# Performance work log

Measured on AMD Instinct MI355X. Metric: run time of the kernel, lower is better.

## Reference

```python
import jax, jax.numpy as jnp
import numpy as np

MARGIN = 1.0

def setup_inputs() -> dict:
    key = jax.random.key(0)
    k1, k2, k3 = jax.random.split(key, 3)
    B, C, D = 65536, 1000, 512
    x = jax.random.normal(k1, (B, D), dtype=jnp.float32)
    x = x / jnp.linalg.norm(x, axis=1, keepdims=True)  # docstring: ||x||2 = 1
    labels = jax.random.randint(k2, (B,), 0, C, dtype=jnp.int64)
    centers = jax.random.normal(k3, (C, D), dtype=jnp.float32)
    return {"x": x, "labels": labels, "centers": centers}

def reference(x, labels, centers):
    # l2Norm applied to the centers (module is only used when l2Norm is truthy)
    c = centers / jnp.linalg.norm(centers, axis=1, keepdims=True)  # (C, D)
    # cosine distance to every center: one batched GEMM instead of per-sample loop
    dist = 1.0 - jnp.einsum("bd,cd->bc", x, c)                      # (B, C)
    pos = jnp.take_along_axis(dist, labels[:, None], axis=1)[:, 0]  # (B,)
    # min over all classes != label: mask own class with +inf
    same = jnp.arange(c.shape[0])[None, :] == labels[:, None]       # (B, C)
    neg = jnp.min(jnp.where(same, jnp.inf, dist), axis=1)           # (B,)
    # sum of per-sample hinge losses divided by batch size == mean
    return jnp.mean(jax.nn.relu(pos + MARGIN - neg))
```

## Files before the change

kernel.cpp:

```cpp
#include <hip/hip_runtime.h>
#include <stdint.h>

typedef short v8s __attribute__((ext_vector_type(8)));
typedef short v4s __attribute__((ext_vector_type(4)));
typedef float v4f __attribute__((ext_vector_type(4)));

#define BM 256
#define BN 128
#define BKH 32
#define ASH (BM * BKH)
#define TSH ((BM + BN) * BKH)
#define POS_INF __builtin_inff()

typedef __attribute__((address_space(3))) unsigned int lds_uint;
typedef const __attribute__((address_space(1))) unsigned int glb_uint;

__device__ __forceinline__ void load16_lds(const void* g, void* l) {
    __builtin_amdgcn_global_load_lds((glb_uint*)g, (lds_uint*)l, 16, 0, 0);
}

__device__ __forceinline__ short f2bf(float f) {
    uint32_t u = __builtin_bit_cast(uint32_t, f);
    u += 0x7fffu + ((u >> 16) & 1u);
    return (short)(u >> 16);
}

__global__ void prep(const float* __restrict__ centers,
                     unsigned short* __restrict__ cbf,
                     int C, int D, int CP, int CB,
                     const float* __restrict__ x,
                     unsigned short* __restrict__ xbf, size_t nx,
                     int* __restrict__ cnt, int NB,
                     float* __restrict__ out) {
    const int b = blockIdx.x;
    const int t = threadIdx.x;
    if (b == 0 && t == 0) out[0] = 0.0f;
    if (b < CB) {
        const int g = b * 256 + t;
        if (g < NB) cnt[g] = 0;
        const int wave = t >> 6, lane = t & 63;
        const int row = b * 4 + wave;
        if (row >= CP) return;
        if (row >= C) {
            v4s z = {0, 0, 0, 0};
            for (int d = lane * 4; d < D; d += 256)
                *(v4s*)&cbf[(size_t)row * D + d] = z;
            return;
        }
        const float* src = centers + (size_t)row * D;
        float ss = 0.0f;
        for (int d = lane * 4; d < D; d += 256) {
            v4f f = *(const v4f*)&src[d];
            ss += f.x * f.x + f.y * f.y + f.z * f.z + f.w * f.w;
        }
        #pragma unroll
        for (int off = 32; off; off >>= 1) ss += __shfl_xor(ss, off, 64);
        const float rn = rsqrtf(ss);
        for (int d = lane * 4; d < D; d += 256) {
            v4f f = *(const v4f*)&src[d];
            v4s s;
            s.x = f2bf(f.x * rn); s.y = f2bf(f.y * rn);
            s.z = f2bf(f.z * rn); s.w = f2bf(f.w * rn);
            *(v4s*)&cbf[(size_t)row * D + d] = s;
        }
    } else {
        const size_t i = ((size_t)(b - CB) * 256 + t) * 8;
        if (i >= nx) return;
        v4f f0 = *(const v4f*)&x[i];
        v4f f1 = *(const v4f*)&x[i + 4];
        v8s s;
        s[0] = f2bf(f0.x); s[1] = f2bf(f0.y); s[2] = f2bf(f0.z); s[3] = f2bf(f0.w);
        s[4] = f2bf(f1.x); s[5] = f2bf(f1.y); s[6] = f2bf(f1.z); s[7] = f2bf(f1.w);
        *(v8s*)&xbf[i] = s;
    }
}

__global__ void __launch_bounds__(512)
gemm_fused(const unsigned short* __restrict__ xbf,
           const unsigned short* __restrict__ cbf,
           const int* __restrict__ labels,
           float* __restrict__ pos, float* __restrict__ partial,
           int* __restrict__ cnt,
           int Bt, int C, int D, int NT, float margin,
           float* __restrict__ out) {
    extern __shared__ short LDS[];

    const int t   = threadIdx.x;
    const int bid = blockIdx.x;
    const int xcd = bid & 7;
    const int per = bid >> 3;
    const int rowblk = (per >> 3) * 8 + xcd;
    const int nt     = per & 7;
    const int row0 = rowblk * BM;
    const int n0   = nt * BN;

    const int lane = t & 63;
    const int wave = t >> 6;
    const int wm = wave >> 1;
    const int wn = wave & 1;
    const int l15 = lane & 15, q = lane >> 4;

    const int rsub = lane >> 2;
    const int csrc = (lane & 3) ^ ((lane >> 3) & 3);

    int myLab = 0;
    if (t < BM) myLab = labels[row0 + t];

    v4f acc[4][4];
    #pragma unroll
    for (int i = 0; i < 4; ++i)
        #pragma unroll
        for (int j = 0; j < 4; ++j)
            acc[i][j] = (v4f){0.f, 0.f, 0.f, 0.f};

    #define WAITVM3() do { asm volatile("s_waitcnt vmcnt(3)" ::: "memory"); } while (0)
    #define WAITVM0() do { asm volatile("s_waitcnt vmcnt(0)" ::: "memory"); } while (0)
    #define BARRIER() do { __builtin_amdgcn_s_barrier(); \
                           __builtin_amdgcn_sched_barrier(0); } while (0)

    #define STAGE(buf_, k0_) do {                                            \
        load16_lds(&xbf[(size_t)(row0 + wave * 32 + rsub) * D + (k0_) + csrc * 8], \
                   &LDS[(buf_) + (wave * 32) * BKH]);                        \
        load16_lds(&xbf[(size_t)(row0 + wave * 32 + 16 + rsub) * D + (k0_) + csrc * 8], \
                   &LDS[(buf_) + (wave * 32 + 16) * BKH]);                   \
        load16_lds(&cbf[(size_t)(n0 + wave * 16 + rsub) * D + (k0_) + csrc * 8], \
                   &LDS[(buf_) + ASH + (wave * 16) * BKH]);                  \
    } while (0)

    #define TILE(buf_) do {                                                  \
        v8s a[4], b[4];                                                      \
        _Pragma("unroll")                                                    \
        for (int i = 0; i < 4; ++i)                                          \
            a[i] = *(const v8s*)&LDS[(buf_) + (wm * 64 + i * 16 + l15) * BKH \
                                     + ((q ^ ((l15 >> 1) & 3)) << 3)];       \
        _Pragma("unroll")                                                    \
        for (int j = 0; j < 4; ++j)                                          \
            b[j] = *(const v8s*)&LDS[(buf_) + ASH + (wn * 64 + j * 16 + l15) * BKH \
                                     + ((q ^ ((l15 >> 1) & 3)) << 3)];       \
        _Pragma("unroll")                                                    \
        for (int i = 0; i < 4; ++i)                                          \
            _Pragma("unroll")                                                \
            for (int j = 0; j < 4; ++j)                                      \
                acc[i][j] = __builtin_amdgcn_mfma_f32_16x16x32_bf16(         \
                    a[i], b[j], acc[i][j], 0, 0, 0);                         \
    } while (0)

    int bc = 0, b1 = TSH, b2 = 2 * TSH;

    STAGE(bc, 0);
    STAGE(b1, BKH);

    const int KT = D / BKH;
    for (int kt = 0; kt + 2 < KT; ++kt) {
        WAITVM3();
        BARRIER();
        STAGE(b2, (kt + 2) * BKH);
        TILE(bc);
        const int tmp = bc; bc = b1; b1 = b2; b2 = tmp;
    }
    WAITVM3();
    BARRIER();
    TILE(bc);
    WAITVM0();
    BARRIER();
    TILE(b1);

    #undef STAGE
    #undef TILE
    #undef WAITVM3
    #undef WAITVM0
    #undef BARRIER

    __syncthreads();

    int*   Ls    = (int*)LDS;
    float* sMinW = (float*)((char*)LDS + 1024);
    int*   sLast = (int*)((char*)LDS + 3072);
    float* wsum  = (float*)((char*)LDS + 3088);
    if (t < BM) Ls[t] = myLab;
    __syncthreads();

    #pragma unroll
    for (int i = 0; i < 4; ++i) {
        #pragma unroll
        for (int rg = 0; rg < 4; ++rg) {
            const int row_l = wm * 64 + i * 16 + q * 4 + rg;
            const int lab = Ls[row_l];
            float m = POS_INF;
            #pragma unroll
            for (int j = 0; j < 4; ++j) {
                const int col = n0 + wn * 64 + j * 16 + l15;
                const float d = 1.0f - acc[i][j][rg];
                if (col == lab)
                    __hip_atomic_store(&pos[row0 + row_l], d,
                                       __ATOMIC_RELAXED, __HIP_MEMORY_SCOPE_AGENT);
                else if (col < C) m = fminf(m, d);
            }
            m = fminf(m, __shfl_xor(m, 1, 64));
            m = fminf(m, __shfl_xor(m, 2, 64));
            m = fminf(m, __shfl_xor(m, 4, 64));
            m = fminf(m, __shfl_xor(m, 8, 64));
            if (l15 == 0) sMinW[wn * BM + row_l] = m;
        }
    }
    __syncthreads();
    if (t < BM) {
        const float m = fminf(sMinW[t], sMinW[BM + t]);
        __hip_atomic_store(&partial[(size_t)nt * Bt + row0 + t], m,
                           __ATOMIC_RELAXED, __HIP_MEMORY_SCOPE_AGENT);
    }
    __syncthreads();

    if (t == 0) {
        __builtin_amdgcn_s_waitcnt(0);
        const int old = __hip_atomic_fetch_add(&cnt[rowblk], 1,
                                               __ATOMIC_RELAXED,
                                               __HIP_MEMORY_SCOPE_AGENT);
        *sLast = (old == NT - 1);
    }
    __syncthreads();
    if (!*sLast) return;

    float hng = 0.0f;
    if (t < BM) {
        const int r = row0 + t;
        float neg = POS_INF;
        for (int tt = 0; tt < NT; ++tt)
            neg = fminf(neg, __hip_atomic_load(&partial[(size_t)tt * Bt + r],
                                               __ATOMIC_RELAXED,
                                               __HIP_MEMORY_SCOPE_AGENT));
        const float p = __hip_atomic_load(&pos[r], __ATOMIC_RELAXED,
                                          __HIP_MEMORY_SCOPE_AGENT);
        hng = fmaxf(0.0f, p + margin - neg);
    }
    #pragma unroll
    for (int off = 32; off; off >>= 1) hng += __shfl_down(hng, off, 64);
    if (lane == 0) wsum[wave] = hng;
    __syncthreads();
    if (t == 0) {
        float s = 0.0f;
        #pragma unroll
        for (int w = 0; w < 8; ++w) s += wsum[w];
        atomicAdd(out, s * (1.0f / (float)Bt));
    }
}

extern "C" void kernel_launch(void* const* d_in, const int* in_sizes, int n_in,
                              void* d_out, int out_size, void* d_ws, size_t ws_size,
                              hipStream_t stream) {
    const float* x       = (const float*)d_in[0];
    const int*   labels  = (const int*)d_in[1];
    const float* centers = (const float*)d_in[2];
    float* out = (float*)d_out;

    const int Bt = in_sizes[1];
    const int D  = in_sizes[0] / Bt;
    const int C  = in_sizes[2] / D;
    const int NT = (C + BN - 1) / BN;
    const int CP = NT * BN;
    const int NB = Bt / BM;

    char* ws = (char*)d_ws;
    unsigned short* cbf = (unsigned short*)ws;
    size_t off = (size_t)CP * D * 2;
    off = (off + 255) & ~(size_t)255;
    float* pos = (float*)(ws + off);      off += (size_t)Bt * 4;
    float* partial = (float*)(ws + off);  off += (size_t)NT * Bt * 4;
    int* cnt = (int*)(ws + off);          off += (size_t)NB * 4;
    off = (off + 255) & ~(size_t)255;
    unsigned short* xbf = (unsigned short*)(ws + off);

    const size_t nx = (size_t)Bt * D;
    const int CB = CP / 4;
    const int XB = (int)((nx / 8 + 255) / 256);
    prep<<<CB + XB, 256, 0, stream>>>(centers, cbf, C, D, CP, CB, x, xbf, nx,
                                      cnt, NB, out);

    static bool lds_attr_set = false;
    if (!lds_attr_set) {
        hipFuncSetAttribute(reinterpret_cast<const void*>(gemm_fused),
                            hipFuncAttributeMaxDynamicSharedMemorySize,
                            3 * TSH * (int)sizeof(short));
        lds_attr_set = true;
    }
    gemm_fused<<<NB * NT, 512, 3 * TSH * sizeof(short), stream>>>(
        xbf, cbf, labels, pos, partial, cnt, Bt, C, D, NT, 1.0f, out);
}
```

Measured before the change: 285.0 us.

## Fuse x fp32-to-bf16 conversion into GEMM tile loads, drop separate prep pass

The standalone conversion of x to bf16 is removed. The GEMM now streams fp32 x rows straight into LDS with a swizzled layout and converts them to bf16 in registers using v_cvt_pk_bf16_f32 before the MFMAs. The pipeline shrinks from three LDS buffers to two, waiting on vmcnt(0) each iteration. This saves a 64K x 512 read and write round trip through the workspace. In exchange, each of the 8 column-tile blocks reads twice the A bytes from global memory and spends extra ALU on conversion, and prefetch overlap gets shallower.

```diff
diff --git a/kernel.cpp b/kernel.cpp
--- a/kernel.cpp
+++ b/kernel.cpp
@@ -8,8 +8,9 @@
 #define BM 256
 #define BN 128
 #define BKH 32
-#define ASH (BM * BKH)
-#define TSH ((BM + BN) * BKH)
+#define ABUF_SH (BM * 2 * BKH)
+#define BBUF_SH (BN * BKH)
+#define TSH (ABUF_SH + BBUF_SH)
 #define POS_INF __builtin_inff()
 
 typedef __attribute__((address_space(3))) unsigned int lds_uint;
@@ -28,55 +29,42 @@
 __global__ void prep(const float* __restrict__ centers,
                      unsigned short* __restrict__ cbf,
                      int C, int D, int CP, int CB,
-                     const float* __restrict__ x,
-                     unsigned short* __restrict__ xbf, size_t nx,
                      int* __restrict__ cnt, int NB,
                      float* __restrict__ out) {
     const int b = blockIdx.x;
     const int t = threadIdx.x;
     if (b == 0 && t == 0) out[0] = 0.0f;
-    if (b < CB) {
-        const int g = b * 256 + t;
-        if (g < NB) cnt[g] = 0;
-        const int wave = t >> 6, lane = t & 63;
-        const int row = b * 4 + wave;
-        if (row >= CP) return;
-        if (row >= C) {
-            v4s z = {0, 0, 0, 0};
-            for (int d = lane * 4; d < D; d += 256)
-                *(v4s*)&cbf[(size_t)row * D + d] = z;
-            return;
-        }
-        const float* src = centers + (size_t)row * D;
-        float ss = 0.0f;
-        for (int d = lane * 4; d < D; d += 256) {
-            v4f f = *(const v4f*)&src[d];
-            ss += f.x * f.x + f.y * f.y + f.z * f.z + f.w * f.w;
-        }
-        #pragma unroll
-        for (int off = 32; off; off >>= 1) ss += __shfl_xor(ss, off, 64);
-        const float rn = rsqrtf(ss);
-        for (int d = lane * 4; d < D; d += 256) {
-            v4f f = *(const v4f*)&src[d];
-            v4s s;
-            s.x = f2bf(f.x * rn); s.y = f2bf(f.y * rn);
-            s.z = f2bf(f.z * rn); s.w = f2bf(f.w * rn);
-            *(v4s*)&cbf[(size_t)row * D + d] = s;
-        }
-    } else {
-        const size_t i = ((size_t)(b - CB) * 256 + t) * 8;
-        if (i >= nx) return;
-        v4f f0 = *(const v4f*)&x[i];
-        v4f f1 = *(const v4f*)&x[i + 4];
-        v8s s;
-        s[0] = f2bf(f0.x); s[1] = f2bf(f0.y); s[2] = f2bf(f0.z); s[3] = f2bf(f0.w);
-        s[4] = f2bf(f1.x); s[5] = f2bf(f1.y); s[6] = f2bf(f1.z); s[7] = f2bf(f1.w);
-        *(v8s*)&xbf[i] = s;
+    const int g = b * 256 + t;
+    if (g < NB) cnt[g] = 0;
+    const int wave = t >> 6, lane = t & 63;
+    const int row = b * 4 + wave;
+    if (row >= CP) return;
+    if (row >= C) {
+        v4s z = {0, 0, 0, 0};
+        for (int d = lane * 4; d < D; d += 256)
+            *(v4s*)&cbf[(size_t)row * D + d] = z;
+        return;
+    }
+    const float* src = centers + (size_t)row * D;
+    float ss = 0.0f;
+    for (int d = lane * 4; d < D; d += 256) {
+        v4f f = *(const v4f*)&src[d];
+        ss += f.x * f.x + f.y * f.y + f.z * f.z + f.w * f.w;
+    }
+    #pragma unroll
+    for (int off = 32; off; off >>= 1) ss += __shfl_xor(ss, off, 64);
+    const float rn = rsqrtf(ss);
+    for (int d = lane * 4; d < D; d += 256) {
+        v4f f = *(const v4f*)&src[d];
+        v4s s;
+        s.x = f2bf(f.x * rn); s.y = f2bf(f.y * rn);
+        s.z = f2bf(f.z * rn); s.w = f2bf(f.w * rn);
+        *(v4s*)&cbf[(size_t)row * D + d] = s;
     }
 }
 
 __global__ void __launch_bounds__(512)
-gemm_fused(const unsigned short* __restrict__ xbf,
+gemm_fused(const float* __restrict__ x,
            const unsigned short* __restrict__ cbf,
            const int* __restrict__ labels,
            float* __restrict__ pos, float* __restrict__ partial,
@@ -100,9 +88,6 @@
     const int wn = wave & 1;
     const int l15 = lane & 15, q = lane >> 4;
 
-    const int rsub = lane >> 2;
-    const int csrc = (lane & 3) ^ ((lane >> 3) & 3);
-
     int myLab = 0;
     if (t < BM) myLab = labels[row0 + t];
 
@@ -113,30 +98,48 @@
         for (int j = 0; j < 4; ++j)
             acc[i][j] = (v4f){0.f, 0.f, 0.f, 0.f};
 
-    #define WAITVM3() do { asm volatile("s_waitcnt vmcnt(3)" ::: "memory"); } while (0)
     #define WAITVM0() do { asm volatile("s_waitcnt vmcnt(0)" ::: "memory"); } while (0)
     #define BARRIER() do { __builtin_amdgcn_s_barrier(); \
                            __builtin_amdgcn_sched_barrier(0); } while (0)
 
     #define STAGE(buf_, k0_) do {                                            \
-        load16_lds(&xbf[(size_t)(row0 + wave * 32 + rsub) * D + (k0_) + csrc * 8], \
-                   &LDS[(buf_) + (wave * 32) * BKH]);                        \
-        load16_lds(&xbf[(size_t)(row0 + wave * 32 + 16 + rsub) * D + (k0_) + csrc * 8], \
-                   &LDS[(buf_) + (wave * 32 + 16) * BKH]);                   \
-        load16_lds(&cbf[(size_t)(n0 + wave * 16 + rsub) * D + (k0_) + csrc * 8], \
-                   &LDS[(buf_) + ASH + (wave * 16) * BKH]);                  \
+        _Pragma("unroll")                                                    \
+        for (int p = 0; p < 4; ++p) {                                        \
+            const int gA_ = (lane & 7) ^ ((p * 4 + (lane >> 4)) & 7);        \
+            load16_lds(&x[(size_t)(row0 + wave * 32 + p * 8 + (lane >> 3)) * D \
+                          + (k0_) + gA_ * 4],                                \
+                       &LDS[(buf_) + (wave * 32 + p * 8) * 64]);             \
+        }                                                                    \
+        load16_lds(&cbf[(size_t)(n0 + wave * 16 + (lane >> 2)) * D + (k0_)   \
+                        + (((lane & 3) ^ ((lane >> 3) & 3)) * 8)],           \
+                   &LDS[(buf_) + ABUF_SH + (wave * 16) * BKH]);              \
     } while (0)
 
     #define TILE(buf_) do {                                                  \
         v8s a[4], b[4];                                                      \
-        _Pragma("unroll")                                                    \
-        for (int i = 0; i < 4; ++i)                                          \
-            a[i] = *(const v8s*)&LDS[(buf_) + (wm * 64 + i * 16 + l15) * BKH \
+        const float* Af_ = (const float*)&LDS[(buf_)];                       \
+        _Pragma("unroll")                                                    \
+        for (int j = 0; j < 4; ++j)                                          \
+            b[j] = *(const v8s*)&LDS[(buf_) + ABUF_SH                        \
+                                     + (wn * 64 + j * 16 + l15) * BKH        \
                                      + ((q ^ ((l15 >> 1) & 3)) << 3)];       \
         _Pragma("unroll")                                                    \
-        for (int j = 0; j < 4; ++j)                                          \
-            b[j] = *(const v8s*)&LDS[(buf_) + ASH + (wn * 64 + j * 16 + l15) * BKH \
-                                     + ((q ^ ((l15 >> 1) & 3)) << 3)];       \
+        for (int i = 0; i < 4; ++i) {                                        \
+            const int m_ = wm * 64 + i * 16 + l15;                           \
+            const int h_ = l15 >> 1;                                         \
+            v4f f0 = *(const v4f*)&Af_[m_ * 32 + (((2 * q) ^ h_) << 2)];     \
+            v4f f1 = *(const v4f*)&Af_[m_ * 32 + (((2 * q + 1) ^ h_) << 2)]; \
+            union { v8s s; uint32_t u[4]; } au;                              \
+            asm("v_cvt_pk_bf16_f32 %0, %1, %2"                               \
+                : "=v"(au.u[0]) : "v"(f0.x), "v"(f0.y));                     \
+            asm("v_cvt_pk_bf16_f32 %0, %1, %2"                               \
+                : "=v"(au.u[1]) : "v"(f0.z), "v"(f0.w));                     \
+            asm("v_cvt_pk_bf16_f32 %0, %1, %2"                               \
+                : "=v"(au.u[2]) : "v"(f1.x), "v"(f1.y));                     \
+            asm("v_cvt_pk_bf16_f32 %0, %1, %2"                               \
+                : "=v"(au.u[3]) : "v"(f1.z), "v"(f1.w));                     \
+            a[i] = au.s;                                                     \
+        }                                                                    \
         _Pragma("unroll")                                                    \
         for (int i = 0; i < 4; ++i)                                          \
             _Pragma("unroll")                                                \
@@ -145,29 +148,21 @@
                     a[i], b[j], acc[i][j], 0, 0, 0);                         \
     } while (0)
 
-    int bc = 0, b1 = TSH, b2 = 2 * TSH;
+    int bc = 0, bnx = TSH;
 
     STAGE(bc, 0);
-    STAGE(b1, BKH);
 
     const int KT = D / BKH;
-    for (int kt = 0; kt + 2 < KT; ++kt) {
-        WAITVM3();
+    for (int kt = 0; kt < KT; ++kt) {
+        WAITVM0();
         BARRIER();
-        STAGE(b2, (kt + 2) * BKH);
+        if (kt + 1 < KT) STAGE(bnx, (kt + 1) * BKH);
         TILE(bc);
-        const int tmp = bc; bc = b1; b1 = b2; b2 = tmp;
-    }
-    WAITVM3();
-    BARRIER();
-    TILE(bc);
-    WAITVM0();
-    BARRIER();
-    TILE(b1);
+        const int tmp = bc; bc = bnx; bnx = tmp;
+    }
 
     #undef STAGE
     #undef TILE
-    #undef WAITVM3
     #undef WAITVM0
     #undef BARRIER
 
@@ -267,22 +262,17 @@
     float* pos = (float*)(ws + off);      off += (size_t)Bt * 4;
     float* partial = (float*)(ws + off);  off += (size_t)NT * Bt * 4;
     int* cnt = (int*)(ws + off);          off += (size_t)NB * 4;
-    off = (off + 255) & ~(size_t)255;
-    unsigned short* xbf = (unsigned short*)(ws + off);
-
-    const size_t nx = (size_t)Bt * D;
+
     const int CB = CP / 4;
-    const int XB = (int)((nx / 8 + 255) / 256);
-    prep<<<CB + XB, 256, 0, stream>>>(centers, cbf, C, D, CP, CB, x, xbf, nx,
-                                      cnt, NB, out);
+    prep<<<CB, 256, 0, stream>>>(centers, cbf, C, D, CP, CB, cnt, NB, out);
 
     static bool lds_attr_set = false;
     if (!lds_attr_set) {
         hipFuncSetAttribute(reinterpret_cast<const void*>(gemm_fused),
                             hipFuncAttributeMaxDynamicSharedMemorySize,
-                            3 * TSH * (int)sizeof(short));
+                            2 * TSH * (int)sizeof(short));
         lds_attr_set = true;
     }
-    gemm_fused<<<NB * NT, 512, 3 * TSH * sizeof(short), stream>>>(
-        xbf, cbf, labels, pos, partial, cnt, Bt, C, D, NT, 1.0f, out);
-}
+    gemm_fused<<<NB * NT, 512, 2 * TSH * sizeof(short), stream>>>(
+        x, cbf, labels, pos, partial, cnt, Bt, C, D, NT, 1.0f, out);
+}
```

New measurement: 292.3 us. 2.5% more time.
